# Optimization experiments

Hardware: AMD Instinct MI355X
Metric: run time of the kernel (lower is better)

Reference implementation:

```python
import jax, jax.numpy as jnp
import numpy as np

K = 16  # num_neighbors
L = 3   # stacked PointTransformer layers


def _mlp2(x, w1, b1, w2, b2):
    return jax.nn.relu(x @ w1 + b1) @ w2 + b2


def setup_inputs() -> dict:
    key = jax.random.key(0)
    ks = jax.random.split(key, 10)
    B, N, D = 2, 8192, 3
    HP, HA = 32, 12  # pos_mlp hidden, attn_mlp hidden (3*4)
    f = lambda k, shp, s: jax.random.normal(k, shp, dtype=jnp.float32) * s
    return {
        "feats": f(ks[0], (B, N, D), 1.0),
        "pos": f(ks[1], (B, N, 3), 1.0),
        "mask": jnp.ones((B, N), dtype=bool),  # unused by PT.forward
        "w_qkv": f(ks[2], (L, D, 3 * D), 1.0 / np.sqrt(D)),
        "pos_w1": f(ks[3], (L, 3, HP), 1.0 / np.sqrt(3.0)),
        "pos_b1": jnp.zeros((L, HP), jnp.float32),
        "pos_w2": f(ks[4], (L, HP, D), 1.0 / np.sqrt(HP)),
        "pos_b2": jnp.zeros((L, D), jnp.float32),
        "attn_w1": f(ks[5], (L, D, HA), 1.0 / np.sqrt(D)),
        "attn_b1": jnp.zeros((L, HA), jnp.float32),
        "attn_w2": f(ks[6], (L, HA, D), 1.0 / np.sqrt(HA)),
        "attn_b2": jnp.zeros((L, D), jnp.float32),
        "lin_w": f(ks[7], (D, 2), 1.0 / np.sqrt(D)),
        "lin_b": jnp.zeros((2,), jnp.float32),
    }


def reference(feats, pos, mask, w_qkv, pos_w1, pos_b1, pos_w2, pos_b2,
              attn_w1, attn_b1, attn_w2, attn_b2, lin_w, lin_b):
    # kNN indices from pairwise squared distances (monotonic in the norm the
    # original uses, so topk-smallest gives identical neighbor sets).
    sq = jnp.sum(pos * pos, axis=-1)                               # [B,N]
    d2 = sq[:, :, None] + sq[:, None, :] - 2.0 * jnp.einsum('bic,bjc->bij', pos, pos)
    _, idx = jax.lax.top_k(-d2, K)                                 # [B,N,K]

    gather = jax.vmap(lambda t, i: t[i])                           # [B,N,d],[B,N,K]->[B,N,K,d]
    pos_j = gather(pos, idx)                                       # [B,N,K,3]
    rel_pos = pos[:, :, None, :] - pos_j                           # [B,N,K,3]

    h = feats
    for l in range(L):
        qkv = h @ w_qkv[l]                                         # [B,N,9]
        q, k, v = jnp.split(qkv, 3, axis=-1)
        k_j = gather(k, idx)                                       # [B,N,K,3]
        v_j = gather(v, idx)
        rel_emb = _mlp2(rel_pos, pos_w1[l], pos_b1[l], pos_w2[l], pos_b2[l])
        qk_rel = q[:, :, None, :] - k_j
        sim = _mlp2(qk_rel + rel_emb, attn_w1[l], attn_b1[l], attn_w2[l], attn_b2[l])
        attn = jax.nn.softmax(sim, axis=-2)                        # softmax over neighbors
        agg = jnp.einsum('bijd,bijd->bid', attn, v_j + rel_emb)    # [B,N,3]
        h = jax.nn.sigmoid(agg)
    out = h @ lin_w + lin_b                                        # [B,N,2]
    return jax.nn.softmax(out, axis=2)
```

## Files before the change

kernel.cpp:

```cpp
#include <hip/hip_runtime.h>
#include <math.h>

#define N_PTS 8192
#define BATCH 2
#define KNB 16
#define NQ (BATCH * N_PTS)

#define H    0.35f
#define INVH (1.0f / 0.35f)
#define NC   30
#define LBOX (0.5f * H * NC)
#define NCELL (NC * NC * NC)
#define MCELL (2 * NCELL)
#define NROW1 9
#define NROWT 43
#define NCHK 8
#define CHKP (N_PTS / NCHK)
#define SCANG 8192
#define MERGG 1024
#define WCAP 8192

typedef unsigned long long u64;

__device__ __forceinline__ float med3f(float a, float b, float c) {
#if __has_builtin(__builtin_amdgcn_fmed3f)
    return __builtin_amdgcn_fmed3f(a, b, c);
#else
    return fmaxf(fminf(a, b), fminf(fmaxf(a, b), c));
#endif
}

__device__ __forceinline__ unsigned sortable(float x) {
    unsigned u = __float_as_uint(x);
    return u ^ ((unsigned)((int)u >> 31) | 0x80000000u);
}

__device__ __forceinline__ void ins_u64(u64 (&pk)[KNB], u64 key) {
    if (key < pk[0]) {
#pragma unroll
        for (int s = 0; s < KNB; ++s) {
            const u64 ds1 = (s < KNB - 1) ? pk[s + 1] : 0ull;
            const bool c0 = key < pk[s];
            const bool c1 = key < ds1;
            pk[s] = c1 ? ds1 : (c0 ? key : pk[s]);
        }
    }
}

__device__ __forceinline__ void sort16_desc_u64(u64 (&a)[KNB]) {
#pragma unroll
    for (int k = 2; k <= 16; k <<= 1) {
#pragma unroll
        for (int j = k >> 1; j > 0; j >>= 1) {
#pragma unroll
            for (int i = 0; i < 16; ++i) {
                const int l = i ^ j;
                if (l > i) {
                    const bool dirDesc = ((i & k) == 0);
                    const u64 mx = a[i] > a[l] ? a[i] : a[l];
                    const u64 mn = a[i] > a[l] ? a[l] : a[i];
                    a[i] = dirDesc ? mx : mn;
                    a[l] = dirDesc ? mn : mx;
                }
            }
        }
    }
}

__device__ __forceinline__ void merge64_u64(u64 (&pk)[KNB]) {
#pragma unroll
    for (int mm = 1; mm <= 32; mm <<= 1) {
        u64 L[KNB];
#pragma unroll
        for (int i = 0; i < KNB; ++i) {
            const u64 a = pk[i];
            const u64 c = __shfl_xor(pk[KNB - 1 - i], mm);
            L[i] = a < c ? a : c;
        }
#pragma unroll
        for (int dd = 8; dd >= 1; dd >>= 1) {
#pragma unroll
            for (int i = 0; i < KNB; ++i) {
                if ((i & dd) == 0) {
                    const u64 hi = L[i] > L[i | dd] ? L[i] : L[i | dd];
                    const u64 lo = L[i] > L[i | dd] ? L[i | dd] : L[i];
                    L[i] = hi; L[i | dd] = lo;
                }
            }
        }
#pragma unroll
        for (int i = 0; i < KNB; ++i) pk[i] = L[i];
    }
}

__global__ __launch_bounds__(256) void kzero(int* __restrict__ p, int n) {
    const int i = blockIdx.x * 256 + threadIdx.x;
    if (i < n) p[i] = 0;
}

__global__ __launch_bounds__(256) void kcount(const float* __restrict__ pos,
                                              int* __restrict__ cnt,
                                              int* __restrict__ cellid) {
    const int g = blockIdx.x * 256 + threadIdx.x;
    const int b = g >> 13;
    const float x = pos[g * 3 + 0], y = pos[g * 3 + 1], z = pos[g * 3 + 2];
    int cx = (int)floorf((x + LBOX) * INVH); cx = min(max(cx, 0), NC - 1);
    int cy = (int)floorf((y + LBOX) * INVH); cy = min(max(cy, 0), NC - 1);
    int cz = (int)floorf((z + LBOX) * INVH); cz = min(max(cz, 0), NC - 1);
    const int c = (((b * NC) + cz) * NC + cy) * NC + cx;
    cellid[g] = c;
    atomicAdd(&cnt[c], 1);
}

__global__ __launch_bounds__(1024) void kscan1(const int* __restrict__ cnt,
                                               int* __restrict__ scanned,
                                               int* __restrict__ bsum) {
    __shared__ int sh[1024];
    const int t = threadIdx.x;
    const int idx = blockIdx.x * 1024 + t;
    int v = (idx < MCELL) ? cnt[idx] : 0;
    sh[t] = v;
    __syncthreads();
    for (int off = 1; off < 1024; off <<= 1) {
        const int add = (t >= off) ? sh[t - off] : 0;
        __syncthreads();
        sh[t] += add;
        __syncthreads();
    }
    if (idx < MCELL) scanned[idx] = sh[t];
    if (t == 1023) bsum[blockIdx.x] = sh[1023];
}

__global__ __launch_bounds__(1024) void kscan2(const int* __restrict__ scanned,
                                               const int* __restrict__ bsum,
                                               int* __restrict__ cell_start) {
    __shared__ int soff;
    const int t = threadIdx.x;
    const int blk = blockIdx.x;
    const int idx = blk * 1024 + t;
    if (t == 0) {
        int s = 0;
        for (int k = 0; k < blk; ++k) s += bsum[k];
        soff = s;
    }
    __syncthreads();
    if (idx < MCELL) cell_start[idx + 1] = scanned[idx] + soff;
    if (idx == 0) cell_start[0] = 0;
}

__global__ __launch_bounds__(256) void kscatter(const float* __restrict__ pos,
                                                const int* __restrict__ cellid,
                                                const int* __restrict__ cell_start,
                                                int* __restrict__ cnt2,
                                                float4* __restrict__ spp,
                                                int* __restrict__ sidx) {
    const int g = blockIdx.x * 256 + threadIdx.x;
    const int c = cellid[g];
    const int off = atomicAdd(&cnt2[c], 1);
    const int p = cell_start[c] + off;
    const float x = pos[g * 3 + 0], y = pos[g * 3 + 1], z = pos[g * 3 + 2];
    spp[p] = make_float4(-2.f * x, -2.f * y, -2.f * z, fmaf(x, x, fmaf(y, y, z * z)));
    sidx[p] = g & (N_PTS - 1);
}

__global__ __launch_bounds__(64) void ksearch_fast(const float4* __restrict__ spp,
                                                   const int* __restrict__ sidx,
                                                   const int* __restrict__ cs,
                                                   int* __restrict__ knn,
                                                   int* __restrict__ ovf_list,
                                                   int* __restrict__ ovf_cnt) {
    __shared__ int rst[4][NROWT], ren[4][NROWT];
    const int tid = threadIdx.x;
    const int li  = tid & 15;
    const int gq  = tid >> 4;
    const int sq  = blockIdx.x * 4 + gq;
    const int b   = sq >> 13;

    for (int t = tid; t < 4 * NROWT; t += 64) {
        const int q = t / NROWT, r = t % NROWT;
        const int sq2 = blockIdx.x * 4 + q;
        const int b2  = sq2 >> 13;
        const float4 m2 = spp[sq2];
        const float px = -0.5f * m2.x, py = -0.5f * m2.y, pz = -0.5f * m2.z;
        int c2x = (int)floorf((px + LBOX) * INVH); c2x = min(max(c2x, 0), NC - 1);
        int c2y = (int)floorf((py + LBOX) * INVH); c2y = min(max(c2y, 0), NC - 1);
        int c2z = (int)floorf((pz + LBOX) * INVH); c2z = min(max(c2z, 0), NC - 1);

        int st = 0, en = 0;
        int z, y, xlo, xhi;
        bool ok = true;
        if (r < NROW1) {
            z = c2z + r / 3 - 1;
            y = c2y + (r % 3) - 1;
            xlo = max(c2x - 1, 0); xhi = min(c2x + 1, NC - 1);
        } else {
            const int rr = r - NROW1;
            if (rr < 10) {
                z = c2z + (rr < 5 ? -2 : 2);
                y = c2y + (rr % 5) - 2;
                xlo = max(c2x - 2, 0); xhi = min(c2x + 2, NC - 1);
            } else if (rr < 16) {
                const int k = rr - 10;
                z = c2z + (k % 3) - 1;
                y = c2y + (k < 3 ? -2 : 2);
                xlo = max(c2x - 2, 0); xhi = min(c2x + 2, NC - 1);
            } else {
                const int k = rr - 16;
                const int m = k % 9;
                z = c2z + m / 3 - 1;
                y = c2y + (m % 3) - 1;
                const int xx = c2x + (k < 9 ? -2 : 2);
                xlo = xhi = xx;
                ok = (xx >= 0) && (xx < NC);
            }
        }
        if (ok && z >= 0 && z < NC && y >= 0 && y < NC) {
            const int rowb = (((b2 * NC) + z) * NC + y) * NC;
            st = cs[rowb + xlo];
            en = cs[rowb + xhi + 1];
        }
        rst[q][r] = st; ren[q][r] = en;
    }
    __syncthreads();

    const float4 me = spp[sq];
    const float qx = -0.5f * me.x, qy = -0.5f * me.y, qz = -0.5f * me.z;
    const float qsq = me.w;
    int cx = (int)floorf((qx + LBOX) * INVH); cx = min(max(cx, 0), NC - 1);
    int cy = (int)floorf((qy + LBOX) * INVH); cy = min(max(cy, 0), NC - 1);
    int cz = (int)floorf((qz + LBOX) * INVH); cz = min(max(cz, 0), NC - 1);

    float d[KNB];
#pragma unroll
    for (int k = 0; k < KNB; ++k) d[k] = 3.4e38f;

    auto scan1_rows = [&](int r0, int r1) {
        for (int r = r0; r < r1; ++r) {
            const int st = rst[gq][r], en = ren[gq][r];
            for (int p = st + li; p < en; p += 16) {
                const float4 v = spp[p];
                const float x = fmaf(qx, v.x, fmaf(qy, v.y, fmaf(qz, v.z, v.w)));
#pragma unroll
                for (int s = 0; s < KNB - 1; ++s) d[s] = med3f(d[s], d[s + 1], x);
                d[KNB - 1] = fminf(d[KNB - 1], x);
            }
        }
    };

    auto boundtest = [&](int R) -> bool {
        const float bxl = fmaf((float)(cx - R), H, -LBOX);
        const float bxh = fmaf((float)(cx + R + 1), H, -LBOX);
        const float byl = fmaf((float)(cy - R), H, -LBOX);
        const float byh = fmaf((float)(cy + R + 1), H, -LBOX);
        const float bzl = fmaf((float)(cz - R), H, -LBOX);
        const float bzh = fmaf((float)(cz + R + 1), H, -LBOX);
        const float m = fminf(fminf(fminf(qx - bxl, bxh - qx),
                                    fminf(qy - byl, byh - qy)),
                              fminf(qz - bzl, bzh - qz));
        if (!(m > 0.f)) return false;
        const float Bf = fmaf(m, m, -1e-4f) - qsq;
        int c = 0;
#pragma unroll
        for (int k = 0; k < KNB; ++k) c += (d[k] <= Bf) ? 1 : 0;
#pragma unroll
        for (int off = 1; off < 16; off <<= 1) c += __shfl_xor(c, off);
        return c >= KNB;
    };

    scan1_rows(0, NROW1);
    const bool done1 = boundtest(1);
    bool ovf = false;
    if (!done1) {
        scan1_rows(NROW1, NROWT);
        if (!boundtest(2)) ovf = true;
    }
    if (ovf) {
        if (li == 0) { const int s2 = atomicAdd(ovf_cnt, 1); ovf_list[s2] = sq; }
        return;
    }
    const int nrows = done1 ? NROW1 : NROWT;

#pragma unroll
    for (int mm = 1; mm <= 8; mm <<= 1) {
        float L[KNB];
#pragma unroll
        for (int i = 0; i < KNB; ++i)
            L[i] = fminf(d[i], __shfl_xor(d[KNB - 1 - i], mm));
#pragma unroll
        for (int dd = 8; dd >= 1; dd >>= 1) {
#pragma unroll
            for (int i = 0; i < KNB; ++i) {
                if ((i & dd) == 0) {
                    const float hi = fmaxf(L[i], L[i | dd]);
                    const float lo = fminf(L[i], L[i | dd]);
                    L[i] = hi; L[i | dd] = lo;
                }
            }
        }
#pragma unroll
        for (int i = 0; i < KNB; ++i) d[i] = L[i];
    }
    const float thr = d[0];

    u64 pk[KNB];
#pragma unroll
    for (int k = 0; k < KNB; ++k) pk[k] = 0xFFFFFFFFFFFFFFFFull;

    for (int r = 0; r < nrows; ++r) {
        const int st = rst[gq][r], en = ren[gq][r];
        for (int p = st + li; p < en; p += 16) {
            const float4 v = spp[p];
            const float x = fmaf(qx, v.x, fmaf(qy, v.y, fmaf(qz, v.z, v.w)));
            if (x <= thr) {
                ins_u64(pk, ((u64)sortable(x) << 32) | (unsigned)sidx[p]);
            }
        }
    }

#pragma unroll
    for (int mm = 1; mm <= 8; mm <<= 1) {
        u64 L[KNB];
#pragma unroll
        for (int i = 0; i < KNB; ++i) {
            const u64 a = pk[i];
            const u64 c = __shfl_xor(pk[KNB - 1 - i], mm);
            L[i] = a < c ? a : c;
        }
#pragma unroll
        for (int dd = 8; dd >= 1; dd >>= 1) {
#pragma unroll
            for (int i = 0; i < KNB; ++i) {
                if ((i & dd) == 0) {
                    const u64 hi = L[i] > L[i | dd] ? L[i] : L[i | dd];
                    const u64 lo = L[i] > L[i | dd] ? L[i | dd] : L[i];
                    L[i] = hi; L[i | dd] = lo;
                }
            }
        }
#pragma unroll
        for (int i = 0; i < KNB; ++i) pk[i] = L[i];
    }

    const int qorig = sidx[sq];
    const int obase = ((b << 13) + qorig) * KNB;
    u64 sel = pk[0];
#pragma unroll
    for (int s = 1; s < KNB; ++s) sel = (li == s) ? pk[s] : sel;
    knn[obase + li] = (int)(unsigned)(sel & 0xFFFFFFFFull);
}

__global__ __launch_bounds__(64, 4) void kslow_scan(const float4* __restrict__ spp,
                                                    const int* __restrict__ sidx,
                                                    const int* __restrict__ ovf_list,
                                                    const int* __restrict__ ovf_cnt,
                                                    u64* __restrict__ pbuf) {
    const int lane = threadIdx.x;
    const int ntask = min(*ovf_cnt, WCAP) * NCHK;

    for (int task = blockIdx.x; task < ntask; task += SCANG) {
        const int w = task >> 3;
        const int c = task & (NCHK - 1);
        const int sq = ovf_list[w];
        const int b  = sq >> 13;
        const float4 me = spp[sq];
        const float qx = -0.5f * me.x, qy = -0.5f * me.y, qz = -0.5f * me.z;
        const int cbase = (b << 13) + c * CHKP;

        u64 pk[KNB];
#pragma unroll
        for (int t0 = 0; t0 < 2; ++t0) {
            const int tb = cbase + lane + t0 * 512;
            float4 v[8];
            int id[8];
#pragma unroll
            for (int u = 0; u < 8; ++u) v[u] = spp[tb + u * 64];
#pragma unroll
            for (int u = 0; u < 8; ++u) id[u] = sidx[tb + u * 64];
#pragma unroll
            for (int u = 0; u < 8; ++u) {
                const float x = fmaf(qx, v[u].x, fmaf(qy, v[u].y, fmaf(qz, v[u].z, v[u].w)));
                pk[t0 * 8 + u] = ((u64)sortable(x) << 32) | (unsigned)id[u];
            }
        }

        sort16_desc_u64(pk);
        merge64_u64(pk);

        u64 sel = pk[0];
#pragma unroll
        for (int s = 1; s < KNB; ++s) sel = (lane == s) ? pk[s] : sel;
        if (lane < KNB) pbuf[(size_t)task * KNB + lane] = sel;
    }
}

__global__ __launch_bounds__(64) void kslow_merge(const float4* __restrict__ spp,
                                                  const int* __restrict__ sidx,
                                                  int* __restrict__ knn,
                                                  const int* __restrict__ ovf_list,
                                                  const int* __restrict__ ovf_cnt,
                                                  const u64* __restrict__ pbuf) {
    const int lane = threadIdx.x;
    const int nov = *ovf_cnt;

    for (int w = blockIdx.x; w < nov; w += MERGG) {
        const int sq = ovf_list[w];
        const int b  = sq >> 13;

        u64 pk[KNB];
#pragma unroll
        for (int k = 0; k < KNB; ++k) pk[k] = 0xFFFFFFFFFFFFFFFFull;

        if (w < WCAP) {
            const u64 a0 = pbuf[(size_t)w * (NCHK * KNB) + lane];
            const u64 a1 = pbuf[(size_t)w * (NCHK * KNB) + 64 + lane];
            ins_u64(pk, a0);
            ins_u64(pk, a1);
        } else {
            const float4 me = spp[sq];
            const float qx = -0.5f * me.x, qy = -0.5f * me.y, qz = -0.5f * me.z;
            const int base = b << 13;
            unsigned smax = 0xFFFFFFFFu;
            for (int t = lane; t < N_PTS; t += 64) {
                const float4 v = spp[base + t];
                const float x = fmaf(qx, v.x, fmaf(qy, v.y, fmaf(qz, v.z, v.w)));
                const unsigned sx = sortable(x);
                if (sx <= smax) {
                    ins_u64(pk, ((u64)sx << 32) | (unsigned)sidx[base + t]);
                    smax = (unsigned)(pk[0] >> 32);
                }
            }
        }

        merge64_u64(pk);

        const int qorig = sidx[sq];
        const int obase = ((b << 13) + qorig) * KNB;
        u64 sel = pk[0];
#pragma unroll
        for (int s = 1; s < KNB; ++s) sel = (lane == s) ? pk[s] : sel;
        if (lane < KNB) knn[obase + lane] = (int)(unsigned)(sel & 0xFFFFFFFFull);
    }
}

__global__ __launch_bounds__(256) void pt_layer_f(const float* __restrict__ hin,
                                                  const float* __restrict__ pos,
                                                  const int* __restrict__ knn,
                                                  const float* __restrict__ wqkv,
                                                  const float* __restrict__ pw1,
                                                  const float* __restrict__ pb1,
                                                  const float* __restrict__ pw2,
                                                  const float* __restrict__ pb2,
                                                  const float* __restrict__ aw1,
                                                  const float* __restrict__ ab1,
                                                  const float* __restrict__ aw2,
                                                  const float* __restrict__ ab2,
                                                  float* __restrict__ hout,
                                                  const float* __restrict__ lw,
                                                  const float* __restrict__ lb,
                                                  float* __restrict__ out,
                                                  int last) {
    const int gt = blockIdx.x * 256 + threadIdx.x;
    const int qg = gt >> 4;
    const int j  = gt & 15;
    const int b  = qg >> 13;
    const int jj = knn[qg * KNB + j] & (N_PTS - 1);
    const int g  = (b << 13) + jj;

    const float hi0 = hin[qg * 3 + 0], hi1 = hin[qg * 3 + 1], hi2 = hin[qg * 3 + 2];
    const float hj0 = hin[g * 3 + 0],  hj1 = hin[g * 3 + 1],  hj2 = hin[g * 3 + 2];
    const float rx = pos[qg * 3 + 0] - pos[g * 3 + 0];
    const float ry = pos[qg * 3 + 1] - pos[g * 3 + 1];
    const float rz = pos[qg * 3 + 2] - pos[g * 3 + 2];

    const float q0 = fmaf(hi0, wqkv[0], fmaf(hi1, wqkv[9],  hi2 * wqkv[18]));
    const float q1 = fmaf(hi0, wqkv[1], fmaf(hi1, wqkv[10], hi2 * wqkv[19]));
    const float q2 = fmaf(hi0, wqkv[2], fmaf(hi1, wqkv[11], hi2 * wqkv[20]));
    const float k0 = fmaf(hj0, wqkv[3], fmaf(hj1, wqkv[12], hj2 * wqkv[21]));
    const float k1 = fmaf(hj0, wqkv[4], fmaf(hj1, wqkv[13], hj2 * wqkv[22]));
    const float k2 = fmaf(hj0, wqkv[5], fmaf(hj1, wqkv[14], hj2 * wqkv[23]));
    const float v0 = fmaf(hj0, wqkv[6], fmaf(hj1, wqkv[15], hj2 * wqkv[24]));
    const float v1 = fmaf(hj0, wqkv[7], fmaf(hj1, wqkv[16], hj2 * wqkv[25]));
    const float v2 = fmaf(hj0, wqkv[8], fmaf(hj1, wqkv[17], hj2 * wqkv[26]));

    float e0 = pb2[0], e1 = pb2[1], e2 = pb2[2];
#pragma unroll
    for (int hh = 0; hh < 32; ++hh) {
        float t = fmaf(rx, pw1[hh], fmaf(ry, pw1[32 + hh], fmaf(rz, pw1[64 + hh], pb1[hh])));
        t = fmaxf(t, 0.0f);
        e0 = fmaf(t, pw2[hh * 3 + 0], e0);
        e1 = fmaf(t, pw2[hh * 3 + 1], e1);
        e2 = fmaf(t, pw2[hh * 3 + 2], e2);
    }

    const float x0 = q0 - k0 + e0;
    const float x1 = q1 - k1 + e1;
    const float x2 = q2 - k2 + e2;

    float s0 = ab2[0], s1 = ab2[1], s2 = ab2[2];
#pragma unroll
    for (int hh = 0; hh < 12; ++hh) {
        float t = fmaf(x0, aw1[hh], fmaf(x1, aw1[12 + hh], fmaf(x2, aw1[24 + hh], ab1[hh])));
        t = fmaxf(t, 0.0f);
        s0 = fmaf(t, aw2[hh * 3 + 0], s0);
        s1 = fmaf(t, aw2[hh * 3 + 1], s1);
        s2 = fmaf(t, aw2[hh * 3 + 2], s2);
    }

    const float w0 = v0 + e0, w1 = v1 + e1, w2 = v2 + e2;

    float m0 = s0, m1 = s1, m2 = s2;
#pragma unroll
    for (int off = 1; off < 16; off <<= 1) {
        m0 = fmaxf(m0, __shfl_xor(m0, off));
        m1 = fmaxf(m1, __shfl_xor(m1, off));
        m2 = fmaxf(m2, __shfl_xor(m2, off));
    }
    const float ex0 = __expf(s0 - m0), ex1 = __expf(s1 - m1), ex2 = __expf(s2 - m2);
    float n0 = ex0 * w0, n1 = ex1 * w1, n2 = ex2 * w2;
    float den0 = ex0, den1 = ex1, den2 = ex2;
#pragma unroll
    for (int off = 1; off < 16; off <<= 1) {
        den0 += __shfl_xor(den0, off); n0 += __shfl_xor(n0, off);
        den1 += __shfl_xor(den1, off); n1 += __shfl_xor(n1, off);
        den2 += __shfl_xor(den2, off); n2 += __shfl_xor(n2, off);
    }

    if (j == 0) {
        const float h0 = 1.f / (1.f + __expf(-(n0 / den0)));
        const float h1 = 1.f / (1.f + __expf(-(n1 / den1)));
        const float h2 = 1.f / (1.f + __expf(-(n2 / den2)));
        if (!last) {
            hout[qg * 3 + 0] = h0;
            hout[qg * 3 + 1] = h1;
            hout[qg * 3 + 2] = h2;
        } else {
            const float o0 = fmaf(h0, lw[0], fmaf(h1, lw[2], fmaf(h2, lw[4], lb[0])));
            const float o1 = fmaf(h0, lw[1], fmaf(h1, lw[3], fmaf(h2, lw[5], lb[1])));
            const float mm = fmaxf(o0, o1);
            const float ea = __expf(o0 - mm), eb = __expf(o1 - mm);
            const float inv = 1.f / (ea + eb);
            out[qg * 2 + 0] = ea * inv;
            out[qg * 2 + 1] = eb * inv;
        }
    }
}

extern "C" void kernel_launch(void* const* d_in, const int* in_sizes, int n_in,
                              void* d_out, int out_size, void* d_ws, size_t ws_size,
                              hipStream_t stream) {
    const float* feats = (const float*)d_in[0];
    const float* pos   = (const float*)d_in[1];
    const float* wqkv = (const float*)d_in[3];
    const float* pw1  = (const float*)d_in[4];
    const float* pb1  = (const float*)d_in[5];
    const float* pw2  = (const float*)d_in[6];
    const float* pb2  = (const float*)d_in[7];
    const float* aw1  = (const float*)d_in[8];
    const float* ab1  = (const float*)d_in[9];
    const float* aw2  = (const float*)d_in[10];
    const float* ab2  = (const float*)d_in[11];
    const float* lw   = (const float*)d_in[12];
    const float* lb   = (const float*)d_in[13];
    float* out = (float*)d_out;

    size_t o = 0;
    auto take = [&](size_t bytes) { size_t r = o; o += (bytes + 15) & ~(size_t)15; return r; };
    const size_t o_cnt   = take((size_t)(2 * MCELL + 4) * 4);
    const size_t o_scan  = take((size_t)MCELL * 4);
    const size_t o_cs    = take((size_t)(MCELL + 1) * 4);
    const size_t o_bsum  = take((size_t)256 * 4);
    const size_t o_cid   = take((size_t)NQ * 4);
    const size_t o_spp   = take((size_t)NQ * 16);
    const size_t o_sidx  = take((size_t)NQ * 4);
    const size_t o_knn   = take((size_t)NQ * KNB * 4);
    const size_t o_ovfl  = take((size_t)NQ * 4);
    const size_t o_hA    = take((size_t)NQ * 3 * 4);
    const size_t o_hB    = take((size_t)NQ * 3 * 4);
    const size_t o_pbuf  = take((size_t)WCAP * NCHK * KNB * 8);
    if (ws_size < o) return;

    char* ws = (char*)d_ws;
    int*    cnt     = (int*)(ws + o_cnt);
    int*    cnt2    = cnt + MCELL;
    int*    ovf_cnt = cnt + 2 * MCELL;
    int*    scan  = (int*)(ws + o_scan);
    int*    cs    = (int*)(ws + o_cs);
    int*    bsum  = (int*)(ws + o_bsum);
    int*    cid   = (int*)(ws + o_cid);
    float4* spp   = (float4*)(ws + o_spp);
    int*    sidx  = (int*)(ws + o_sidx);
    int*    knn   = (int*)(ws + o_knn);
    int*    ovfl  = (int*)(ws + o_ovfl);
    float*  hA    = (float*)(ws + o_hA);
    float*  hB    = (float*)(ws + o_hB);
    u64*    pbuf  = (u64*)(ws + o_pbuf);

    const int nscan = (MCELL + 1023) / 1024;

    kzero<<<(2 * MCELL + 1 + 255) / 256, 256, 0, stream>>>(cnt, 2 * MCELL + 1);
    kcount<<<NQ / 256, 256, 0, stream>>>(pos, cnt, cid);
    kscan1<<<nscan, 1024, 0, stream>>>(cnt, scan, bsum);
    kscan2<<<nscan, 1024, 0, stream>>>(scan, bsum, cs);
    kscatter<<<NQ / 256, 256, 0, stream>>>(pos, cid, cs, cnt2, spp, sidx);
    ksearch_fast<<<NQ / 4, 64, 0, stream>>>(spp, sidx, cs, knn, ovfl, ovf_cnt);
    kslow_scan<<<SCANG, 64, 0, stream>>>(spp, sidx, ovfl, ovf_cnt, pbuf);
    kslow_merge<<<MERGG, 64, 0, stream>>>(spp, sidx, knn, ovfl, ovf_cnt, pbuf);

    pt_layer_f<<<NQ * 16 / 256, 256, 0, stream>>>(feats, pos, knn,
        wqkv + 0, pw1 + 0, pb1 + 0, pw2 + 0, pb2 + 0,
        aw1 + 0, ab1 + 0, aw2 + 0, ab2 + 0,
        hA, lw, lb, out, 0);
    pt_layer_f<<<NQ * 16 / 256, 256, 0, stream>>>(hA, pos, knn,
        wqkv + 27, pw1 + 96, pb1 + 32, pw2 + 96, pb2 + 3,
        aw1 + 36, ab1 + 12, aw2 + 36, ab2 + 3,
        hB, lw, lb, out, 0);
    pt_layer_f<<<NQ * 16 / 256, 256, 0, stream>>>(hB, pos, knn,
        wqkv + 54, pw1 + 192, pb1 + 64, pw2 + 192, pb2 + 6,
        aw1 + 72, ab1 + 24, aw2 + 72, ab2 + 6,
        hB, lw, lb, out, 1);
}
```

Before: 125.6 us.

## Split kNN cell-row scan across two wavefronts per query and merge through LDS

The fast kNN search kernel now uses 128 threads per block, with two wavefronts each scanning half of the neighbor cell rows for the same four queries. The partial top-16 distance lists and packed candidate lists are merged through shared memory using bitonic merges, and block-wide syncs gather the stopping-test counts. This doubles the parallelism per query to cut per-query latency on the search critical path, at the cost of extra syncs, shared-memory traffic and redundant merge work. Separately, the zeroing kernel is replaced with hipMemsetAsync.

```diff
diff --git a/kernel.cpp b/kernel.cpp
--- a/kernel.cpp
+++ b/kernel.cpp
@@ -19,6 +19,7 @@
 #define SCANG 8192
 #define MERGG 1024
 #define WCAP 8192
+#define FINF 3.4e38f
 
 typedef unsigned long long u64;
 
@@ -91,11 +92,6 @@
 #pragma unroll
         for (int i = 0; i < KNB; ++i) pk[i] = L[i];
     }
-}
-
-__global__ __launch_bounds__(256) void kzero(int* __restrict__ p, int n) {
-    const int i = blockIdx.x * 256 + threadIdx.x;
-    if (i < n) p[i] = 0;
 }
 
 __global__ __launch_bounds__(256) void kcount(const float* __restrict__ pos,
@@ -163,22 +159,27 @@
     sidx[p] = g & (N_PTS - 1);
 }
 
-__global__ __launch_bounds__(64) void ksearch_fast(const float4* __restrict__ spp,
-                                                   const int* __restrict__ sidx,
-                                                   const int* __restrict__ cs,
-                                                   int* __restrict__ knn,
-                                                   int* __restrict__ ovf_list,
-                                                   int* __restrict__ ovf_cnt) {
-    __shared__ int rst[4][NROWT], ren[4][NROWT];
+__global__ __launch_bounds__(128, 6) void ksearch_fast(const float4* __restrict__ spp,
+                                                       const int* __restrict__ sidx,
+                                                       const int* __restrict__ cs,
+                                                       int* __restrict__ knn,
+                                                       int* __restrict__ ovf_list,
+                                                       int* __restrict__ ovf_cnt) {
+    __shared__ int rstL[4][NROWT], renL[4][NROWT];
+    __shared__ int shc1[4][2], shc2[4][2];
+    __shared__ float shf[4][2][KNB];
+    __shared__ u64 shp[4][2][KNB];
+
     const int tid = threadIdx.x;
+    const int wv  = tid >> 6;
     const int li  = tid & 15;
-    const int gq  = tid >> 4;
-    const int sq  = blockIdx.x * 4 + gq;
+    const int q   = (tid >> 4) & 3;
+    const int sq  = blockIdx.x * 4 + q;
     const int b   = sq >> 13;
 
-    for (int t = tid; t < 4 * NROWT; t += 64) {
-        const int q = t / NROWT, r = t % NROWT;
-        const int sq2 = blockIdx.x * 4 + q;
+    for (int t = tid; t < 4 * NROWT; t += 128) {
+        const int qq = t / NROWT, r = t % NROWT;
+        const int sq2 = blockIdx.x * 4 + qq;
         const int b2  = sq2 >> 13;
         const float4 m2 = spp[sq2];
         const float px = -0.5f * m2.x, py = -0.5f * m2.y, pz = -0.5f * m2.z;
@@ -219,7 +220,7 @@
             st = cs[rowb + xlo];
             en = cs[rowb + xhi + 1];
         }
-        rst[q][r] = st; ren[q][r] = en;
+        rstL[qq][r] = st; renL[qq][r] = en;
     }
     __syncthreads();
 
@@ -230,55 +231,66 @@
     int cy = (int)floorf((qy + LBOX) * INVH); cy = min(max(cy, 0), NC - 1);
     int cz = (int)floorf((qz + LBOX) * INVH); cz = min(max(cz, 0), NC - 1);
 
-    float d[KNB];
-#pragma unroll
-    for (int k = 0; k < KNB; ++k) d[k] = 3.4e38f;
-
-    auto scan1_rows = [&](int r0, int r1) {
-        for (int r = r0; r < r1; ++r) {
-            const int st = rst[gq][r], en = ren[gq][r];
-            for (int p = st + li; p < en; p += 16) {
-                const float4 v = spp[p];
-                const float x = fmaf(qx, v.x, fmaf(qy, v.y, fmaf(qz, v.z, v.w)));
-#pragma unroll
-                for (int s = 0; s < KNB - 1; ++s) d[s] = med3f(d[s], d[s + 1], x);
-                d[KNB - 1] = fminf(d[KNB - 1], x);
-            }
-        }
-    };
-
-    auto boundtest = [&](int R) -> bool {
+    auto boxm = [&](int R) -> float {
         const float bxl = fmaf((float)(cx - R), H, -LBOX);
         const float bxh = fmaf((float)(cx + R + 1), H, -LBOX);
         const float byl = fmaf((float)(cy - R), H, -LBOX);
         const float byh = fmaf((float)(cy + R + 1), H, -LBOX);
         const float bzl = fmaf((float)(cz - R), H, -LBOX);
         const float bzh = fmaf((float)(cz + R + 1), H, -LBOX);
-        const float m = fminf(fminf(fminf(qx - bxl, bxh - qx),
-                                    fminf(qy - byl, byh - qy)),
-                              fminf(qz - bzl, bzh - qz));
-        if (!(m > 0.f)) return false;
-        const float Bf = fmaf(m, m, -1e-4f) - qsq;
+        return fminf(fminf(fminf(qx - bxl, bxh - qx),
+                           fminf(qy - byl, byh - qy)),
+                     fminf(qz - bzl, bzh - qz));
+    };
+
+    float d[KNB];
+#pragma unroll
+    for (int k = 0; k < KNB; ++k) d[k] = FINF;
+
+    auto scan1_rows = [&](int r0, int r1) {
+        for (int r = r0; r < r1; ++r) {
+            const int st = rstL[q][r], en = renL[q][r];
+            for (int p = st + li; p < en; p += 16) {
+                const float4 v = spp[p];
+                const float x = fmaf(qx, v.x, fmaf(qy, v.y, fmaf(qz, v.z, v.w)));
+#pragma unroll
+                for (int s = 0; s < KNB - 1; ++s) d[s] = med3f(d[s], d[s + 1], x);
+                d[KNB - 1] = fminf(d[KNB - 1], x);
+            }
+        }
+    };
+    auto count16 = [&](float Bf) -> int {
         int c = 0;
 #pragma unroll
         for (int k = 0; k < KNB; ++k) c += (d[k] <= Bf) ? 1 : 0;
 #pragma unroll
         for (int off = 1; off < 16; off <<= 1) c += __shfl_xor(c, off);
-        return c >= KNB;
+        return c;
     };
 
-    scan1_rows(0, NROW1);
-    const bool done1 = boundtest(1);
-    bool ovf = false;
-    if (!done1) {
-        scan1_rows(NROW1, NROWT);
-        if (!boundtest(2)) ovf = true;
-    }
-    if (ovf) {
-        if (li == 0) { const int s2 = atomicAdd(ovf_cnt, 1); ovf_list[s2] = sq; }
-        return;
-    }
-    const int nrows = done1 ? NROW1 : NROWT;
+    scan1_rows(wv ? 5 : 0, wv ? NROW1 : 5);
+    const float m1 = boxm(1);
+    const float Bf1 = fmaf(m1, m1, -1e-4f) - qsq;
+    {
+        const int c = count16(Bf1);
+        if (li == 0) shc1[q][wv] = c;
+    }
+    __syncthreads();
+    const bool done1 = (m1 > 0.f) && (shc1[q][0] + shc1[q][1] >= KNB);
+
+    if (!done1) scan1_rows(wv ? 26 : NROW1, wv ? NROWT : 26);
+    const float m2 = boxm(2);
+    const float Bf2 = fmaf(m2, m2, -1e-4f) - qsq;
+    {
+        const int c = count16(Bf2);
+        if (li == 0) shc2[q][wv] = c;
+    }
+    __syncthreads();
+    const bool done2 = done1 || ((m2 > 0.f) && (shc2[q][0] + shc2[q][1] >= KNB));
+    const bool ovf = !done2;
+    if (ovf && wv == 0 && li == 0) {
+        const int s2 = atomicAdd(ovf_cnt, 1); ovf_list[s2] = sq;
+    }
 
 #pragma unroll
     for (int mm = 1; mm <= 8; mm <<= 1) {
@@ -300,21 +312,48 @@
 #pragma unroll
         for (int i = 0; i < KNB; ++i) d[i] = L[i];
     }
+    shf[q][wv][li] = d[li];
+    __syncthreads();
+    {
+        float L[KNB];
+#pragma unroll
+        for (int i = 0; i < KNB; ++i)
+            L[i] = fminf(d[i], shf[q][wv ^ 1][KNB - 1 - i]);
+#pragma unroll
+        for (int dd = 8; dd >= 1; dd >>= 1) {
+#pragma unroll
+            for (int i = 0; i < KNB; ++i) {
+                if ((i & dd) == 0) {
+                    const float hi = fmaxf(L[i], L[i | dd]);
+                    const float lo = fminf(L[i], L[i | dd]);
+                    L[i] = hi; L[i | dd] = lo;
+                }
+            }
+        }
+#pragma unroll
+        for (int i = 0; i < KNB; ++i) d[i] = L[i];
+    }
     const float thr = d[0];
 
     u64 pk[KNB];
 #pragma unroll
     for (int k = 0; k < KNB; ++k) pk[k] = 0xFFFFFFFFFFFFFFFFull;
 
-    for (int r = 0; r < nrows; ++r) {
-        const int st = rst[gq][r], en = ren[gq][r];
-        for (int p = st + li; p < en; p += 16) {
-            const float4 v = spp[p];
-            const float x = fmaf(qx, v.x, fmaf(qy, v.y, fmaf(qz, v.z, v.w)));
-            if (x <= thr) {
-                ins_u64(pk, ((u64)sortable(x) << 32) | (unsigned)sidx[p]);
-            }
-        }
+    if (!ovf) {
+        auto scan2_rows = [&](int r0, int r1) {
+            for (int r = r0; r < r1; ++r) {
+                const int st = rstL[q][r], en = renL[q][r];
+                for (int p = st + li; p < en; p += 16) {
+                    const float4 v = spp[p];
+                    const float x = fmaf(qx, v.x, fmaf(qy, v.y, fmaf(qz, v.z, v.w)));
+                    if (x <= thr) {
+                        ins_u64(pk, ((u64)sortable(x) << 32) | (unsigned)sidx[p]);
+                    }
+                }
+            }
+        };
+        scan2_rows(wv ? 5 : 0, wv ? NROW1 : 5);
+        if (!done1) scan2_rows(wv ? 26 : NROW1, wv ? NROWT : 26);
     }
 
 #pragma unroll
@@ -340,13 +379,35 @@
 #pragma unroll
         for (int i = 0; i < KNB; ++i) pk[i] = L[i];
     }
-
-    const int qorig = sidx[sq];
-    const int obase = ((b << 13) + qorig) * KNB;
-    u64 sel = pk[0];
-#pragma unroll
-    for (int s = 1; s < KNB; ++s) sel = (li == s) ? pk[s] : sel;
-    knn[obase + li] = (int)(unsigned)(sel & 0xFFFFFFFFull);
+    shp[q][wv][li] = pk[li];
+    __syncthreads();
+
+    if (wv == 0 && !ovf) {
+        u64 L[KNB];
+#pragma unroll
+        for (int i = 0; i < KNB; ++i) {
+            const u64 a = pk[i];
+            const u64 c = shp[q][1][KNB - 1 - i];
+            L[i] = a < c ? a : c;
+        }
+#pragma unroll
+        for (int dd = 8; dd >= 1; dd >>= 1) {
+#pragma unroll
+            for (int i = 0; i < KNB; ++i) {
+                if ((i & dd) == 0) {
+                    const u64 hi = L[i] > L[i | dd] ? L[i] : L[i | dd];
+                    const u64 lo = L[i] > L[i | dd] ? L[i | dd] : L[i];
+                    L[i] = hi; L[i | dd] = lo;
+                }
+            }
+        }
+        const int qorig = sidx[sq];
+        const int obase = ((b << 13) + qorig) * KNB;
+        u64 sel = L[0];
+#pragma unroll
+        for (int s = 1; s < KNB; ++s) sel = (li == s) ? L[s] : sel;
+        knn[obase + li] = (int)(unsigned)(sel & 0xFFFFFFFFull);
+    }
 }
 
 __global__ __launch_bounds__(64, 4) void kslow_scan(const float4* __restrict__ spp,
@@ -597,12 +658,12 @@
 
     const int nscan = (MCELL + 1023) / 1024;
 
-    kzero<<<(2 * MCELL + 1 + 255) / 256, 256, 0, stream>>>(cnt, 2 * MCELL + 1);
+    hipMemsetAsync(cnt, 0, (size_t)(2 * MCELL + 1) * 4, stream);
     kcount<<<NQ / 256, 256, 0, stream>>>(pos, cnt, cid);
     kscan1<<<nscan, 1024, 0, stream>>>(cnt, scan, bsum);
     kscan2<<<nscan, 1024, 0, stream>>>(scan, bsum, cs);
     kscatter<<<NQ / 256, 256, 0, stream>>>(pos, cid, cs, cnt2, spp, sidx);
-    ksearch_fast<<<NQ / 4, 64, 0, stream>>>(spp, sidx, cs, knn, ovfl, ovf_cnt);
+    ksearch_fast<<<NQ / 4, 128, 0, stream>>>(spp, sidx, cs, knn, ovfl, ovf_cnt);
     kslow_scan<<<SCANG, 64, 0, stream>>>(spp, sidx, ovfl, ovf_cnt, pbuf);
     kslow_merge<<<MERGG, 64, 0, stream>>>(spp, sidx, knn, ovfl, ovf_cnt, pbuf);
 
```

After: 187.2 us. +49.1%, slower.

## Flatten cell-row scans into prefix-summed candidate stream in kNN search

Applied to the files above, without the earlier changes.

The search kernel now builds a per-query prefix sum of candidate counts across the neighbouring cell rows, so the 16 lanes of each query walk one flat candidate index range instead of looping row by row. This is meant to cut lane idling on short rows. The first-pass top-16 update now skips the med3 insertion chain when a candidate cannot enter the list. The zeroing kernel is replaced with hipMemsetAsync. The flattened loop adds a row-lookup while loop and a serial prefix-sum step done by four threads.

```diff
diff --git a/kernel.cpp b/kernel.cpp
--- a/kernel.cpp
+++ b/kernel.cpp
@@ -19,6 +19,7 @@
 #define SCANG 8192
 #define MERGG 1024
 #define WCAP 8192
+#define FINF 3.4e38f
 
 typedef unsigned long long u64;
 
@@ -91,11 +92,6 @@
 #pragma unroll
         for (int i = 0; i < KNB; ++i) pk[i] = L[i];
     }
-}
-
-__global__ __launch_bounds__(256) void kzero(int* __restrict__ p, int n) {
-    const int i = blockIdx.x * 256 + threadIdx.x;
-    if (i < n) p[i] = 0;
 }
 
 __global__ __launch_bounds__(256) void kcount(const float* __restrict__ pos,
@@ -169,59 +165,69 @@
                                                    int* __restrict__ knn,
                                                    int* __restrict__ ovf_list,
                                                    int* __restrict__ ovf_cnt) {
-    __shared__ int rst[4][NROWT], ren[4][NROWT];
+    __shared__ int rstL[4][NROWT];
+    __shared__ int psL[4][NROWT + 1];
     const int tid = threadIdx.x;
     const int li  = tid & 15;
     const int gq  = tid >> 4;
     const int sq  = blockIdx.x * 4 + gq;
     const int b   = sq >> 13;
 
-    for (int t = tid; t < 4 * NROWT; t += 64) {
-        const int q = t / NROWT, r = t % NROWT;
-        const int sq2 = blockIdx.x * 4 + q;
-        const int b2  = sq2 >> 13;
-        const float4 m2 = spp[sq2];
-        const float px = -0.5f * m2.x, py = -0.5f * m2.y, pz = -0.5f * m2.z;
-        int c2x = (int)floorf((px + LBOX) * INVH); c2x = min(max(c2x, 0), NC - 1);
-        int c2y = (int)floorf((py + LBOX) * INVH); c2y = min(max(c2y, 0), NC - 1);
-        int c2z = (int)floorf((pz + LBOX) * INVH); c2z = min(max(c2z, 0), NC - 1);
-
-        int st = 0, en = 0;
-        int z, y, xlo, xhi;
-        bool ok = true;
-        if (r < NROW1) {
-            z = c2z + r / 3 - 1;
-            y = c2y + (r % 3) - 1;
-            xlo = max(c2x - 1, 0); xhi = min(c2x + 1, NC - 1);
-        } else {
-            const int rr = r - NROW1;
-            if (rr < 10) {
-                z = c2z + (rr < 5 ? -2 : 2);
-                y = c2y + (rr % 5) - 2;
-                xlo = max(c2x - 2, 0); xhi = min(c2x + 2, NC - 1);
-            } else if (rr < 16) {
-                const int k = rr - 10;
-                z = c2z + (k % 3) - 1;
-                y = c2y + (k < 3 ? -2 : 2);
-                xlo = max(c2x - 2, 0); xhi = min(c2x + 2, NC - 1);
+    {
+        __shared__ int cntL[4][NROWT];
+        for (int t = tid; t < 4 * NROWT; t += 64) {
+            const int q = t / NROWT, r = t % NROWT;
+            const int sq2 = blockIdx.x * 4 + q;
+            const int b2  = sq2 >> 13;
+            const float4 m2 = spp[sq2];
+            const float px = -0.5f * m2.x, py = -0.5f * m2.y, pz = -0.5f * m2.z;
+            int c2x = (int)floorf((px + LBOX) * INVH); c2x = min(max(c2x, 0), NC - 1);
+            int c2y = (int)floorf((py + LBOX) * INVH); c2y = min(max(c2y, 0), NC - 1);
+            int c2z = (int)floorf((pz + LBOX) * INVH); c2z = min(max(c2z, 0), NC - 1);
+
+            int st = 0, en = 0;
+            int z, y, xlo, xhi;
+            bool ok = true;
+            if (r < NROW1) {
+                z = c2z + r / 3 - 1;
+                y = c2y + (r % 3) - 1;
+                xlo = max(c2x - 1, 0); xhi = min(c2x + 1, NC - 1);
             } else {
-                const int k = rr - 16;
-                const int m = k % 9;
-                z = c2z + m / 3 - 1;
-                y = c2y + (m % 3) - 1;
-                const int xx = c2x + (k < 9 ? -2 : 2);
-                xlo = xhi = xx;
-                ok = (xx >= 0) && (xx < NC);
-            }
-        }
-        if (ok && z >= 0 && z < NC && y >= 0 && y < NC) {
-            const int rowb = (((b2 * NC) + z) * NC + y) * NC;
-            st = cs[rowb + xlo];
-            en = cs[rowb + xhi + 1];
-        }
-        rst[q][r] = st; ren[q][r] = en;
-    }
-    __syncthreads();
+                const int rr = r - NROW1;
+                if (rr < 10) {
+                    z = c2z + (rr < 5 ? -2 : 2);
+                    y = c2y + (rr % 5) - 2;
+                    xlo = max(c2x - 2, 0); xhi = min(c2x + 2, NC - 1);
+                } else if (rr < 16) {
+                    const int k = rr - 10;
+                    z = c2z + (k % 3) - 1;
+                    y = c2y + (k < 3 ? -2 : 2);
+                    xlo = max(c2x - 2, 0); xhi = min(c2x + 2, NC - 1);
+                } else {
+                    const int k = rr - 16;
+                    const int m = k % 9;
+                    z = c2z + m / 3 - 1;
+                    y = c2y + (m % 3) - 1;
+                    const int xx = c2x + (k < 9 ? -2 : 2);
+                    xlo = xhi = xx;
+                    ok = (xx >= 0) && (xx < NC);
+                }
+            }
+            if (ok && z >= 0 && z < NC && y >= 0 && y < NC) {
+                const int rowb = (((b2 * NC) + z) * NC + y) * NC;
+                st = cs[rowb + xlo];
+                en = cs[rowb + xhi + 1];
+            }
+            rstL[q][r] = st; cntL[q][r] = en - st;
+        }
+        __syncthreads();
+        if (tid < 4) {
+            int acc = 0;
+            psL[tid][0] = 0;
+            for (int r = 0; r < NROWT; ++r) { acc += cntL[tid][r]; psL[tid][r + 1] = acc; }
+        }
+        __syncthreads();
+    }
 
     const float4 me = spp[sq];
     const float qx = -0.5f * me.x, qy = -0.5f * me.y, qz = -0.5f * me.z;
@@ -230,22 +236,27 @@
     int cy = (int)floorf((qy + LBOX) * INVH); cy = min(max(cy, 0), NC - 1);
     int cz = (int)floorf((qz + LBOX) * INVH); cz = min(max(cz, 0), NC - 1);
 
+    const int tot1 = psL[gq][NROW1];
+    const int tot2 = psL[gq][NROWT];
+
     float d[KNB];
 #pragma unroll
-    for (int k = 0; k < KNB; ++k) d[k] = 3.4e38f;
-
-    auto scan1_rows = [&](int r0, int r1) {
-        for (int r = r0; r < r1; ++r) {
-            const int st = rst[gq][r], en = ren[gq][r];
-            for (int p = st + li; p < en; p += 16) {
-                const float4 v = spp[p];
-                const float x = fmaf(qx, v.x, fmaf(qy, v.y, fmaf(qz, v.z, v.w)));
-#pragma unroll
-                for (int s = 0; s < KNB - 1; ++s) d[s] = med3f(d[s], d[s + 1], x);
-                d[KNB - 1] = fminf(d[KNB - 1], x);
-            }
-        }
-    };
+    for (int k = 0; k < KNB; ++k) d[k] = FINF;
+
+    int row = 0;
+    int t = li;
+#pragma unroll 4
+    for (; t < tot1; t += 16) {
+        while (t >= psL[gq][row + 1]) ++row;
+        const int p = rstL[gq][row] + (t - psL[gq][row]);
+        const float4 v = spp[p];
+        const float x = fmaf(qx, v.x, fmaf(qy, v.y, fmaf(qz, v.z, v.w)));
+        if (x < d[0]) {
+#pragma unroll
+            for (int s = 0; s < KNB - 1; ++s) d[s] = med3f(d[s], d[s + 1], x);
+            d[KNB - 1] = fminf(d[KNB - 1], x);
+        }
+    }
 
     auto boundtest = [&](int R) -> bool {
         const float bxl = fmaf((float)(cx - R), H, -LBOX);
@@ -267,18 +278,28 @@
         return c >= KNB;
     };
 
-    scan1_rows(0, NROW1);
     const bool done1 = boundtest(1);
     bool ovf = false;
     if (!done1) {
-        scan1_rows(NROW1, NROWT);
+#pragma unroll 4
+        for (; t < tot2; t += 16) {
+            while (t >= psL[gq][row + 1]) ++row;
+            const int p = rstL[gq][row] + (t - psL[gq][row]);
+            const float4 v = spp[p];
+            const float x = fmaf(qx, v.x, fmaf(qy, v.y, fmaf(qz, v.z, v.w)));
+            if (x < d[0]) {
+#pragma unroll
+                for (int s = 0; s < KNB - 1; ++s) d[s] = med3f(d[s], d[s + 1], x);
+                d[KNB - 1] = fminf(d[KNB - 1], x);
+            }
+        }
         if (!boundtest(2)) ovf = true;
     }
     if (ovf) {
         if (li == 0) { const int s2 = atomicAdd(ovf_cnt, 1); ovf_list[s2] = sq; }
         return;
     }
-    const int nrows = done1 ? NROW1 : NROWT;
+    const int tot = done1 ? tot1 : tot2;
 
 #pragma unroll
     for (int mm = 1; mm <= 8; mm <<= 1) {
@@ -306,14 +327,15 @@
 #pragma unroll
     for (int k = 0; k < KNB; ++k) pk[k] = 0xFFFFFFFFFFFFFFFFull;
 
-    for (int r = 0; r < nrows; ++r) {
-        const int st = rst[gq][r], en = ren[gq][r];
-        for (int p = st + li; p < en; p += 16) {
-            const float4 v = spp[p];
-            const float x = fmaf(qx, v.x, fmaf(qy, v.y, fmaf(qz, v.z, v.w)));
-            if (x <= thr) {
-                ins_u64(pk, ((u64)sortable(x) << 32) | (unsigned)sidx[p]);
-            }
+    row = 0;
+#pragma unroll 4
+    for (int t2 = li; t2 < tot; t2 += 16) {
+        while (t2 >= psL[gq][row + 1]) ++row;
+        const int p = rstL[gq][row] + (t2 - psL[gq][row]);
+        const float4 v = spp[p];
+        const float x = fmaf(qx, v.x, fmaf(qy, v.y, fmaf(qz, v.z, v.w)));
+        if (x <= thr) {
+            ins_u64(pk, ((u64)sortable(x) << 32) | (unsigned)sidx[p]);
         }
     }
 
@@ -597,7 +619,7 @@
 
     const int nscan = (MCELL + 1023) / 1024;
 
-    kzero<<<(2 * MCELL + 1 + 255) / 256, 256, 0, stream>>>(cnt, 2 * MCELL + 1);
+    hipMemsetAsync(cnt, 0, (size_t)(2 * MCELL + 1) * 4, stream);
     kcount<<<NQ / 256, 256, 0, stream>>>(pos, cnt, cid);
     kscan1<<<nscan, 1024, 0, stream>>>(cnt, scan, bsum);
     kscan2<<<nscan, 1024, 0, stream>>>(scan, bsum, cs);
```

After: 131.4 us. +4.7%, slower.
